# Optimization experiments

Measured on AMD Instinct MI355X. Metric: run time of the kernel, lower is better.

Reference implementation:

```python
import jax, jax.numpy as jnp
import numpy as np
from jax import lax

NPG = 61      # nodes (electrodes) per graph, hard-coded by 61*hidden reshape
B = 128       # graphs per batch
L = 160       # raw signal length -> final conv length 1
NF = 64       # num_features
HC = 128      # hidden_channels
NCLS = 4


def setup_inputs() -> dict:
    key = jax.random.key(0)
    ks = jax.random.split(key, 16)
    N = B * NPG
    # fully-connected (no self-loops) edges within each graph -> 3660 edges/graph
    a = np.repeat(np.arange(NPG), NPG)
    b = np.tile(np.arange(NPG), NPG)
    m = a != b
    sl, dl = a[m], b[m]
    off = (np.arange(B) * NPG)[:, None]
    edge_index = np.stack([(sl[None] + off).ravel(), (dl[None] + off).ravel()]).astype(np.int64)
    batch = np.repeat(np.arange(B), NPG).astype(np.int64)

    def rn(k, shape, fan_in):
        return jax.random.normal(k, shape, jnp.float32) / np.sqrt(fan_in).astype(np.float32)

    return dict(
        x=jax.random.normal(ks[0], (N, L), jnp.float32),
        edge_index=jnp.asarray(edge_index),
        batch=jnp.asarray(batch),
        edge_features=jax.random.normal(ks[1], (edge_index.shape[1], 3), jnp.float32),
        conv_w0=rn(ks[2], (NF, 1, 7), 7.0), conv_b0=jnp.zeros((NF,), jnp.float32),
        conv_w1=rn(ks[3], (NF, NF, 5), NF * 5.0), conv_b1=jnp.zeros((NF,), jnp.float32),
        conv_w2=rn(ks[4], (NF, NF, 3), NF * 3.0), conv_b2=jnp.zeros((NF,), jnp.float32),
        bn1_g=jnp.ones((NF,), jnp.float32), bn1_b=jnp.zeros((NF,), jnp.float32),
        g_w0=rn(ks[5], (NF, HC), float(NF)), g_b0=jnp.zeros((HC,), jnp.float32),
        g_w1=rn(ks[6], (HC, HC), float(HC)), g_b1=jnp.zeros((HC,), jnp.float32),
        g_w2=rn(ks[7], (HC, HC), float(HC)), g_b2=jnp.zeros((HC,), jnp.float32),
        bn2_g=jnp.ones((HC,), jnp.float32), bn2_b=jnp.zeros((HC,), jnp.float32),
        lin_w0=rn(ks[8], (NPG * HC, HC), float(NPG * HC)), lin_b0=jnp.zeros((HC,), jnp.float32),
        lin_w1=rn(ks[9], (HC, HC), float(HC)), lin_b1=jnp.zeros((HC,), jnp.float32),
        lin_w2=rn(ks[10], (HC, NCLS), float(HC)), lin_b2=jnp.zeros((NCLS,), jnp.float32),
        edge_w=rn(ks[11], (3, 1), 3.0), edge_b=jnp.zeros((1,), jnp.float32),
    )


def _conv1d(x, w, b, pad):
    # x: [N, Cin, L], w: [Cout, Cin, K]
    y = lax.conv_general_dilated(x, w, (1,), [(pad, pad)], dimension_numbers=('NCH', 'OIH', 'NCH'))
    return y + b[None, :, None]


def _maxpool7(x):
    n = x.shape[-1] // 7
    return x[..., : n * 7].reshape(x.shape[0], x.shape[1], n, 7).max(-1)


def _bn(x, g, b):
    # BatchNorm1d in training mode: biased batch statistics
    m = x.mean(0)
    v = x.var(0)
    return (x - m) * lax.rsqrt(v + 1e-5) * g + b


def _forward(x, edge_features, conv_w0, conv_b0, conv_w1, conv_b1, conv_w2, conv_b2,
             bn1_g, bn1_b, g_w0, g_b0, g_w1, g_b1, g_w2, g_b2, bn2_g, bn2_b,
             lin_w0, lin_b0, lin_w1, lin_b1, lin_w2, lin_b2, edge_w, edge_b,
             edge_index, batch):
    N = x.shape[0]
    nb = N // NPG  # == batch.max()+1 for contiguous graph layout
    # tanh-gated edge weights
    ew = jnp.tanh(edge_features @ edge_w + edge_b)            # [E, 1]
    # Conv1d feature extractor: [N,1,160] -> [N,NF,1]
    h = x[:, None, :]
    h = _maxpool7(jax.nn.relu(_conv1d(h, conv_w0, conv_b0, 0)))   # [N,NF,22]
    h = jax.nn.relu(_conv1d(h, conv_w1, conv_b1, 2))               # [N,NF,22]
    h = _maxpool7(h)                                               # [N,NF,3]
    h = _conv1d(h, conv_w2, conv_b2, 0)[:, :, 0]                   # [N,NF]
    h = _bn(h, bn1_g, bn1_b)
    # Edge-weighted GCN hops (MyzConv): lin -> gather src -> scale -> scatter-add dst
    src, dst = edge_index[0], edge_index[1]
    for w, bs, act in ((g_w0, g_b0, True), (g_w1, g_b1, True), (g_w2, g_b2, False)):
        hw = h @ w + bs                                            # [N,HC]
        msg = ew * hw[src]                                         # [E,HC]
        h = jax.ops.segment_sum(msg, dst, num_segments=N)
        if act:
            h = jax.nn.relu(h)
    h = _bn(h, bn2_g, bn2_b)
    # MLP classifier over concatenated node features per graph
    h = h.reshape(nb, NPG * HC)
    h = jax.nn.relu(h @ lin_w0 + lin_b0)
    h = jax.nn.relu(h @ lin_w1 + lin_b1)
    h = h @ lin_w2 + lin_b2
    return jax.nn.log_softmax(h, -1), ew.reshape(nb, -1).T


def reference(x, edge_index, batch, edge_features, conv_w0, conv_b0, conv_w1, conv_b1,
              conv_w2, conv_b2, bn1_g, bn1_b, g_w0, g_b0, g_w1, g_b1, g_w2, g_b2,
              bn2_g, bn2_b, lin_w0, lin_b0, lin_w1, lin_b1, lin_w2, lin_b2, edge_w, edge_b):
    return _forward(x, edge_features, conv_w0, conv_b0, conv_w1, conv_b1, conv_w2, conv_b2,
                    bn1_g, bn1_b, g_w0, g_b0, g_w1, g_b1, g_w2, g_b2, bn2_g, bn2_b,
                    lin_w0, lin_b0, lin_w1, lin_b1, lin_w2, lin_b2, edge_w, edge_b,
                    edge_index, batch)
```

## Files before the change

### kernel.cpp

```cpp
#include <hip/hip_runtime.h>
#include <math.h>

#define NPGN 61
#define NGRAPH 128
#define NNODES (NPGN*NGRAPH)
#define EPG 3660

typedef float float4v __attribute__((ext_vector_type(4)));
typedef short bf16x8 __attribute__((ext_vector_type(8)));
typedef unsigned short u16;

__device__ __forceinline__ u16 f2bf(float v){
  union { float f; unsigned u; } x; x.f = v;
  unsigned r = (x.u + 0x7FFFu + ((x.u >> 16) & 1u)) >> 16;
  return (u16)r;
}
__device__ __forceinline__ float bf2f(unsigned u){
  union { unsigned u; float f; } x; x.u = u << 16;
  return x.f;
}

__global__ __launch_bounds__(256) void k_prep(const float* __restrict__ w0,
    const float* __restrict__ w1, const float* __restrict__ w2,
    const float* __restrict__ gw0, const float* __restrict__ gw1, const float* __restrict__ gw2,
    const float* __restrict__ lw0,
    float* __restrict__ w0t, u16* __restrict__ w1b, u16* __restrict__ w2b,
    u16* __restrict__ gwt0, u16* __restrict__ gwt1, u16* __restrict__ gwt2,
    u16* __restrict__ lw0t){
  __shared__ __align__(16) u16 tile[32*132];
  int b = blockIdx.x, tid = threadIdx.x;
  if (b < 290){
    int idx = b*256 + tid;
    if (idx < 20480){
      int f = idx / 320, r = idx - f*320;
      int kk = r >> 6, c = r & 63;
      w1b[idx] = f2bf(w1[f*320 + c*5 + kk]);
    } else if (idx < 32768){
      int j = idx - 20480; w2b[j] = f2bf(w2[j]);
    } else if (idx < 40960){
      int j = idx - 32768; int jj = j >> 6, k = j & 63; gwt0[j] = f2bf(gw0[k*128 + jj]);
    } else if (idx < 57344){
      int j = idx - 40960; int jj = j >> 7, k = j & 127; gwt1[j] = f2bf(gw1[k*128 + jj]);
    } else if (idx < 73728){
      int j = idx - 57344; int jj = j >> 7, k = j & 127; gwt2[j] = f2bf(gw2[k*128 + jj]);
    } else if (idx < 74176){
      int j = idx - 73728; int k = j >> 6, f = j & 63; w0t[j] = w0[f*7 + k];
    }
  } else {
    int bb = b - 290;
    int i = bb >> 2, oq = bb & 3;
    for (int idx = tid; idx < 4096; idx += 256){
      int k = idx >> 5, ol = idx & 31;
      tile[ol*132 + k] = f2bf(lw0[((size_t)i*128 + k)*128 + oq*32 + ol]);
    }
    __syncthreads();
    unsigned* dst = (unsigned*)lw0t;
    for (int idx = tid; idx < 2048; idx += 256){
      int ol = idx >> 6, kw = idx & 63;
      unsigned v = (unsigned)tile[ol*132 + 2*kw] | ((unsigned)tile[ol*132 + 2*kw + 1] << 16);
      dst[((size_t)i*128 + oq*32 + ol)*64 + kw] = v;
    }
  }
}

#define A0T_STR 72
#define C1_STR 40
__global__ __launch_bounds__(256) void k_conv(const float* __restrict__ x,
    const float* __restrict__ w0t, const float* __restrict__ b0,
    const u16* __restrict__ w1b, const float* __restrict__ b1,
    const u16* __restrict__ w2b, const float* __restrict__ b2,
    float* __restrict__ h0, float* __restrict__ stat1p){
  int w = threadIdx.x >> 6, lane = threadIdx.x & 63;
  int tid = threadIdx.x;
  int n = blockIdx.x*4 + w;
  __shared__ __align__(16) u16 a0t_s[4][36*A0T_STR];
  __shared__ __align__(16) u16 a1k_s[4][208];
  __shared__ float hstat[4][128];
  u16* a0t = a0t_s[w];
  u16* a1k = a1k_s[w];

  const float* xrow = x + (size_t)__builtin_amdgcn_readfirstlane(n)*160;

  float w0r[7];
  #pragma unroll
  for (int k = 0; k < 7; k++) w0r[k] = w0t[k*64 + lane];
  float b0f = b0[lane];
  #pragma unroll
  for (int rp = 0; rp < 36; rp++)
    if (rp < 2 || rp >= 24) a0t[rp*A0T_STR + lane] = 0;

  #pragma unroll 2
  for (int qp = 0; qp < 11; qp++){
    float win[20];
    #pragma unroll
    for (int j = 0; j < 20; j++) win[j] = xrow[14*qp + j];
    float m0, m1;
    #pragma unroll
    for (int r = 0; r < 7; r++){
      float s = w0r[0]*win[r];
      #pragma unroll
      for (int k = 1; k < 7; k++) s += w0r[k]*win[r+k];
      m0 = r ? fmaxf(m0, s) : s;
    }
    #pragma unroll
    for (int r = 7; r < 14; r++){
      float s = w0r[0]*win[r];
      #pragma unroll
      for (int k = 1; k < 7; k++) s += w0r[k]*win[r+k];
      m1 = (r > 7) ? fmaxf(m1, s) : s;
    }
    a0t[(2 + 2*qp)*A0T_STR + lane] = f2bf(fmaxf(m0 + b0f, 0.f));
    a0t[(3 + 2*qp)*A0T_STR + lane] = f2bf(fmaxf(m1 + b0f, 0.f));
  }

  int q = lane >> 4, r16 = lane & 15;
  float4v acc[4][2];
  #pragma unroll
  for (int mt = 0; mt < 4; mt++)
    #pragma unroll
    for (int nt = 0; nt < 2; nt++)
      acc[mt][nt] = (float4v){0.f,0.f,0.f,0.f};
  #pragma unroll 1
  for (int ks = 0; ks < 10; ks++){
    int kk = ks >> 1;
    int cbase = (ks & 1)*32 + q*8;
    bf16x8 af[4];
    #pragma unroll
    for (int mt = 0; mt < 4; mt++)
      af[mt] = *(const bf16x8*)(w1b + (16*mt + r16)*320 + ks*32 + q*8);
    bf16x8 bv[2];
    #pragma unroll
    for (int nt = 0; nt < 2; nt++)
      bv[nt] = *(const bf16x8*)(a0t + (r16 + 16*nt + kk)*A0T_STR + cbase);
    #pragma unroll
    for (int mt = 0; mt < 4; mt++)
      #pragma unroll
      for (int nt = 0; nt < 2; nt++)
        acc[mt][nt] = __builtin_amdgcn_mfma_f32_16x16x32_bf16(af[mt], bv[nt], acc[mt][nt], 0, 0, 0);
  }

  u16* c1 = a0t;
  #pragma unroll
  for (int mt = 0; mt < 4; mt++){
    float4 bb = *(const float4*)(b1 + 16*mt + 4*q);
    #pragma unroll
    for (int reg = 0; reg < 4; reg++){
      int m = 16*mt + q*4 + reg;
      float bv_ = ((const float*)&bb)[reg];
      c1[m*C1_STR + r16] = f2bf(fmaxf(acc[mt][0][reg] + bv_, 0.f));
      if (r16 <= 4)
        c1[m*C1_STR + 16 + r16] = f2bf(fmaxf(acc[mt][1][reg] + bv_, 0.f));
    }
  }

  {
    bf16x8 f0 = *(const bf16x8*)(c1 + lane*C1_STR);
    bf16x8 f1 = *(const bf16x8*)(c1 + lane*C1_STR + 8);
    bf16x8 f2 = *(const bf16x8*)(c1 + lane*C1_STR + 16);
    float v[24];
    #pragma unroll
    for (int j = 0; j < 8; j++){
      v[j]    = bf2f((u16)f0[j]);
      v[8+j]  = bf2f((u16)f1[j]);
      v[16+j] = bf2f((u16)f2[j]);
    }
    #pragma unroll
    for (int t = 0; t < 3; t++){
      float m = v[t*7];
      #pragma unroll
      for (int r = 1; r < 7; r++) m = fmaxf(m, v[t*7+r]);
      a1k[lane*3 + t] = f2bf(m);
    }
  }

  float4v acc2[4];
  #pragma unroll
  for (int mt = 0; mt < 4; mt++) acc2[mt] = (float4v){0.f,0.f,0.f,0.f};
  #pragma unroll
  for (int ks = 0; ks < 6; ks++){
    bf16x8 bs = *(const bf16x8*)(a1k + ks*32 + q*8);
    #pragma unroll
    for (int mt = 0; mt < 4; mt++){
      bf16x8 af = *(const bf16x8*)(w2b + (16*mt + r16)*192 + ks*32 + q*8);
      acc2[mt] = __builtin_amdgcn_mfma_f32_16x16x32_bf16(af, bs, acc2[mt], 0, 0, 0);
    }
  }
  if (r16 == 0){
    #pragma unroll
    for (int mt = 0; mt < 4; mt++)
      #pragma unroll
      for (int reg = 0; reg < 4; reg++){
        int f = 16*mt + 4*q + reg;
        float v = acc2[mt][reg] + b2[f];
        h0[(size_t)n*64 + f] = v;
        hstat[w][f] = v;
        hstat[w][64 + f] = v*v;
      }
  }
  __syncthreads();
  if (tid < 128){
    float a = hstat[0][tid] + hstat[1][tid] + hstat[2][tid] + hstat[3][tid];
    atomicAdd(&stat1p[(blockIdx.x & 31)*128 + tid], a);
  }
}

#define EW_STR 72
#define HS_STR 136
#define HWT_STR 72
__global__ __launch_bounds__(512) void k_gnn(const float* __restrict__ h0,
    const float* __restrict__ stat1p,
    const float* __restrict__ bn1g, const float* __restrict__ bn1b,
    const u16* __restrict__ gwt0, const float* __restrict__ gb0,
    const u16* __restrict__ gwt1, const float* __restrict__ gb1,
    const u16* __restrict__ gwt2, const float* __restrict__ gb2,
    const float* __restrict__ ef, const float* __restrict__ eww,
    const float* __restrict__ ewb, float* __restrict__ out2,
    u16* __restrict__ hB, float* __restrict__ stat2p){
  int g = blockIdx.x, tid = threadIdx.x;
  int w = tid >> 6, lane = tid & 63, q = lane >> 4, r16 = lane & 15;
  int dt = w & 3, jh = w >> 2;
  __shared__ u16 hs[64*HS_STR];
  __shared__ u16 hwT[128*HWT_STR];
  __shared__ u16 ewl[64*EW_STR];
  __shared__ float bsc[64], bsh[64];
  __shared__ float st2[256];

  bf16x8 af0[2], af1[4], af2[4];
  #pragma unroll
  for (int ks = 0; ks < 2; ks++)
    af0[ks] = *(const bf16x8*)(gwt0 + (16*w + r16)*64 + ks*32 + q*8);
  #pragma unroll
  for (int ks = 0; ks < 4; ks++)
    af1[ks] = *(const bf16x8*)(gwt1 + (16*w + r16)*128 + ks*32 + q*8);
  #pragma unroll
  for (int ks = 0; ks < 4; ks++)
    af2[ks] = *(const bf16x8*)(gwt2 + (16*w + r16)*128 + ks*32 + q*8);
  float4 b40 = *(const float4*)(gb0 + 16*w + 4*q);
  float4 b41 = *(const float4*)(gb1 + 16*w + 4*q);
  float4 b42 = *(const float4*)(gb2 + 16*w + 4*q);

  if (tid < 64){
    float s = 0.f, s2 = 0.f;
    #pragma unroll
    for (int r = 0; r < 32; r++){
      s  += stat1p[r*128 + tid];
      s2 += stat1p[r*128 + 64 + tid];
    }
    float m = s*(1.f/NNODES), v = s2*(1.f/NNODES) - m*m;
    float sc = rsqrtf(v + 1e-5f)*bn1g[tid];
    bsc[tid] = sc; bsh[tid] = bn1b[tid] - m*sc;
  }
  if (tid < 256) st2[tid] = 0.f;
  {
    unsigned* td = (unsigned*)ewl;
    for (int idx = tid; idx < 64*EW_STR/2; idx += 512) td[idx] = 0;
  }
  {
    unsigned* hsd = (unsigned*)hs;
    for (int idx = tid; idx < 3*(HS_STR/2); idx += 512){
      int rr = 61 + idx/(HS_STR/2), cc = idx%(HS_STR/2);
      hsd[rr*(HS_STR/2) + cc] = 0;
    }
  }
  __syncthreads();

  {
    float v0 = eww[0], v1 = eww[1], v2 = eww[2], bb = ewb[0];
    const float* efg = ef + (size_t)g*EPG*3;
    for (int idx = tid; idx < EPG; idx += 512){
      const float* p = efg + idx*3;
      float v = tanhf(p[0]*v0 + p[1]*v1 + p[2]*v2 + bb);
      int s = idx/60, r = idx - s*60;
      int d = r + (r >= s ? 1 : 0);
      ewl[d*EW_STR + s] = f2bf(v);
      out2[(size_t)idx*128 + g] = v;
    }
  }
  {
    unsigned* hsd = (unsigned*)hs;
    for (int idx = tid; idx < 61*32; idx += 512){
      int i = idx >> 5, kw = idx & 31;
      float2 hv = *(const float2*)(h0 + ((size_t)g*61 + i)*64 + kw*2);
      int k0 = kw*2;
      float a = hv.x*bsc[k0] + bsh[k0];
      float b = hv.y*bsc[k0+1] + bsh[k0+1];
      hsd[i*(HS_STR/2) + kw] = (unsigned)f2bf(a) | ((unsigned)f2bf(b) << 16);
    }
  }
  __syncthreads();
  bf16x8 ewf[2];
  #pragma unroll
  for (int ks = 0; ks < 2; ks++)
    ewf[ks] = *(const bf16x8*)(ewl + (16*dt + r16)*EW_STR + ks*32 + q*8);

  #pragma unroll
  for (int nt = 0; nt < 4; nt++){
    float4v acc = {b40.x, b40.y, b40.z, b40.w};
    #pragma unroll
    for (int ks = 0; ks < 2; ks++){
      bf16x8 bv = *(const bf16x8*)(hs + (nt*16 + r16)*HS_STR + ks*32 + q*8);
      acc = __builtin_amdgcn_mfma_f32_16x16x32_bf16(af0[ks], bv, acc, 0, 0, 0);
    }
    #pragma unroll
    for (int r = 0; r < 4; r++)
      hwT[(16*w + 4*q + r)*HWT_STR + nt*16 + r16] = f2bf(acc[r]);
  }
  __syncthreads();
  #pragma unroll
  for (int nt = 0; nt < 4; nt++){
    int j = (jh*4 + nt)*16;
    float4v acc = {0.f,0.f,0.f,0.f};
    #pragma unroll
    for (int ks = 0; ks < 2; ks++){
      bf16x8 bv = *(const bf16x8*)(hwT + (j + r16)*HWT_STR + ks*32 + q*8);
      acc = __builtin_amdgcn_mfma_f32_16x16x32_bf16(ewf[ks], bv, acc, 0, 0, 0);
    }
    #pragma unroll
    for (int r = 0; r < 4; r++){
      int d = 16*dt + 4*q + r;
      hs[d*HS_STR + j + r16] = f2bf(fmaxf(acc[r], 0.f));
    }
  }
  __syncthreads();

  #pragma unroll
  for (int nt = 0; nt < 4; nt++){
    float4v acc = {b41.x, b41.y, b41.z, b41.w};
    #pragma unroll
    for (int ks = 0; ks < 4; ks++){
      bf16x8 bv = *(const bf16x8*)(hs + (nt*16 + r16)*HS_STR + ks*32 + q*8);
      acc = __builtin_amdgcn_mfma_f32_16x16x32_bf16(af1[ks], bv, acc, 0, 0, 0);
    }
    #pragma unroll
    for (int r = 0; r < 4; r++)
      hwT[(16*w + 4*q + r)*HWT_STR + nt*16 + r16] = f2bf(acc[r]);
  }
  __syncthreads();
  #pragma unroll
  for (int nt = 0; nt < 4; nt++){
    int j = (jh*4 + nt)*16;
    float4v acc = {0.f,0.f,0.f,0.f};
    #pragma unroll
    for (int ks = 0; ks < 2; ks++){
      bf16x8 bv = *(const bf16x8*)(hwT + (j + r16)*HWT_STR + ks*32 + q*8);
      acc = __builtin_amdgcn_mfma_f32_16x16x32_bf16(ewf[ks], bv, acc, 0, 0, 0);
    }
    #pragma unroll
    for (int r = 0; r < 4; r++){
      int d = 16*dt + 4*q + r;
      hs[d*HS_STR + j + r16] = f2bf(fmaxf(acc[r], 0.f));
    }
  }
  __syncthreads();

  #pragma unroll
  for (int nt = 0; nt < 4; nt++){
    float4v acc = {b42.x, b42.y, b42.z, b42.w};
    #pragma unroll
    for (int ks = 0; ks < 4; ks++){
      bf16x8 bv = *(const bf16x8*)(hs + (nt*16 + r16)*HS_STR + ks*32 + q*8);
      acc = __builtin_amdgcn_mfma_f32_16x16x32_bf16(af2[ks], bv, acc, 0, 0, 0);
    }
    #pragma unroll
    for (int r = 0; r < 4; r++)
      hwT[(16*w + 4*q + r)*HWT_STR + nt*16 + r16] = f2bf(acc[r]);
  }
  __syncthreads();
  #pragma unroll
  for (int nt = 0; nt < 4; nt++){
    int j = (jh*4 + nt)*16;
    float4v acc = {0.f,0.f,0.f,0.f};
    #pragma unroll
    for (int ks = 0; ks < 2; ks++){
      bf16x8 bv = *(const bf16x8*)(hwT + (j + r16)*HWT_STR + ks*32 + q*8);
      acc = __builtin_amdgcn_mfma_f32_16x16x32_bf16(ewf[ks], bv, acc, 0, 0, 0);
    }
    float cs = 0.f, cq = 0.f;
    #pragma unroll
    for (int r = 0; r < 4; r++){
      int d = 16*dt + 4*q + r;
      if (d < 61){
        float v = acc[r];
        hB[((size_t)g*61 + d)*128 + j + r16] = f2bf(v);
        cs += v; cq += v*v;
      }
    }
    int col = j + r16;
    atomicAdd(&st2[col], cs);
    atomicAdd(&st2[128 + col], cq);
  }
  __syncthreads();
  if (tid < 256) stat2p[(size_t)tid*128 + g] = st2[tid];
}

#define AS_STR 136
__global__ __launch_bounds__(256) void k_mlp0(const u16* __restrict__ hB,
    const float* __restrict__ stat2p,
    const float* __restrict__ bn2g, const float* __restrict__ bn2b,
    const u16* __restrict__ lw0t, float* __restrict__ y0pre){
  int bi = blockIdx.x; int i = bi >> 2, sub = bi & 3;
  int oh = sub & 1, gh = sub >> 1;
  int tid = threadIdx.x, w = tid >> 6, lane = tid & 63, q = lane >> 4, r16 = lane & 15;
  __shared__ u16 As[64*AS_STR];
  __shared__ float sc2[128], sh2[128];
  if (tid < 128){
    float4v sa = {0,0,0,0}, sb = {0,0,0,0};
    #pragma unroll
    for (int r = 0; r < 32; r++){
      sa += *(const float4v*)(stat2p + (size_t)tid*128 + r*4);
      sb += *(const float4v*)(stat2p + (size_t)(128 + tid)*128 + r*4);
    }
    float s = sa[0]+sa[1]+sa[2]+sa[3], s2 = sb[0]+sb[1]+sb[2]+sb[3];
    float m = s*(1.f/NNODES), v = s2*(1.f/NNODES) - m*m;
    float sc = rsqrtf(v + 1e-5f)*bn2g[tid];
    sc2[tid] = sc; sh2[tid] = bn2b[tid] - m*sc;
  }
  __syncthreads();
  {
    const unsigned* hbd = (const unsigned*)hB;
    unsigned* asd = (unsigned*)As;
    for (int idx = tid; idx < 4096; idx += 256){
      int gg = gh*64 + (idx >> 6), kw = idx & 63;
      unsigned pv = hbd[((size_t)gg*61 + i)*64 + kw];
      int k0 = kw*2;
      float a = bf2f(pv & 0xffffu)*sc2[k0] + sh2[k0];
      float b = bf2f(pv >> 16)*sc2[k0+1] + sh2[k0+1];
      asd[(idx >> 6)*(AS_STR/2) + kw] = (unsigned)f2bf(a) | ((unsigned)f2bf(b) << 16);
    }
  }
  __syncthreads();
  const u16* wbase = lw0t + ((size_t)i*128 + oh*64)*128;
  bf16x8 af[4];
  #pragma unroll
  for (int ks = 0; ks < 4; ks++)
    af[ks] = *(const bf16x8*)(As + (16*w + r16)*AS_STR + ks*32 + q*8);
  #pragma unroll
  for (int nt = 0; nt < 4; nt++){
    float4v acc = {0.f,0.f,0.f,0.f};
    #pragma unroll
    for (int ks = 0; ks < 4; ks++){
      bf16x8 bv = *(const bf16x8*)(wbase + (size_t)(nt*16 + r16)*128 + ks*32 + q*8);
      acc = __builtin_amdgcn_mfma_f32_16x16x32_bf16(af[ks], bv, acc, 0, 0, 0);
    }
    #pragma unroll
    for (int r = 0; r < 4; r++){
      int g = gh*64 + 16*w + 4*q + r;
      atomicAdd(&y0pre[(size_t)g*128 + oh*64 + nt*16 + r16], acc[r]);
    }
  }
}

__global__ __launch_bounds__(128) void k_mlp1(const float* __restrict__ y0pre,
    const float* __restrict__ lb0, const float* __restrict__ W1,
    const float* __restrict__ lb1, const float* __restrict__ W2,
    const float* __restrict__ lb2, float* __restrict__ out){
  int g = blockIdx.x, o = threadIdx.x;
  __shared__ float y0[128], y1[128], red[128];
  y0[o] = fmaxf(y0pre[(size_t)g*128 + o] + lb0[o], 0.f);
  __syncthreads();
  float a = lb1[o];
  #pragma unroll 8
  for (int k = 0; k < 128; k++) a += y0[k]*W1[k*128 + o];
  y1[o] = fmaxf(a, 0.f);
  __syncthreads();
  int c = o & 3, kb = o >> 2;
  float a2 = 0.f;
  #pragma unroll
  for (int j = 0; j < 4; j++){
    int k = kb + 32*j;
    a2 += y1[k]*W2[k*4 + c];
  }
  red[o] = a2;
  __syncthreads();
  #pragma unroll
  for (int off = 64; off >= 4; off >>= 1){
    if (o < off) red[o] += red[o + off];
    __syncthreads();
  }
  if (o == 0){
    float v0 = red[0]+lb2[0], v1 = red[1]+lb2[1], v2 = red[2]+lb2[2], v3 = red[3]+lb2[3];
    float m = fmaxf(fmaxf(v0,v1), fmaxf(v2,v3));
    float lse = m + logf(expf(v0-m)+expf(v1-m)+expf(v2-m)+expf(v3-m));
    out[g*4+0]=v0-lse; out[g*4+1]=v1-lse; out[g*4+2]=v2-lse; out[g*4+3]=v3-lse;
  }
}

extern "C" void kernel_launch(void* const* d_in, const int* in_sizes, int n_in,
                              void* d_out, int out_size, void* d_ws, size_t ws_size,
                              hipStream_t stream){
  const float* x    = (const float*)d_in[0];
  const float* ef   = (const float*)d_in[3];
  const float* cw0  = (const float*)d_in[4];
  const float* cb0  = (const float*)d_in[5];
  const float* cw1  = (const float*)d_in[6];
  const float* cb1  = (const float*)d_in[7];
  const float* cw2  = (const float*)d_in[8];
  const float* cb2  = (const float*)d_in[9];
  const float* bn1g = (const float*)d_in[10];
  const float* bn1b = (const float*)d_in[11];
  const float* gw0  = (const float*)d_in[12];
  const float* gb0  = (const float*)d_in[13];
  const float* gw1  = (const float*)d_in[14];
  const float* gb1  = (const float*)d_in[15];
  const float* gw2  = (const float*)d_in[16];
  const float* gb2  = (const float*)d_in[17];
  const float* bn2g = (const float*)d_in[18];
  const float* bn2b = (const float*)d_in[19];
  const float* lw0  = (const float*)d_in[20];
  const float* lb0  = (const float*)d_in[21];
  const float* lw1  = (const float*)d_in[22];
  const float* lb1  = (const float*)d_in[23];
  const float* lw2  = (const float*)d_in[24];
  const float* lb2  = (const float*)d_in[25];
  const float* eww  = (const float*)d_in[26];
  const float* ewb  = (const float*)d_in[27];
  float* out = (float*)d_out;

  float* ws   = (float*)d_ws;
  float* w1s  = ws;
  float* w2s  = w1s + 10240;
  float* w0t  = w2s + 6144;
  float* gws0 = w0t + 448;
  float* gws1 = gws0 + 4096;
  float* gws2 = gws1 + 8192;
  float* h0   = gws2 + 8192;
  float* hBs  = h0 + 499712;
  float* lw0s = hBs + 499712;
  float* accs = lw0s + 499712;

  u16* w1b    = (u16*)w1s;
  u16* w2b    = (u16*)w2s;
  u16* gwt0   = (u16*)gws0;
  u16* gwt1   = (u16*)gws1;
  u16* gwt2   = (u16*)gws2;
  u16* hB     = (u16*)hBs;
  u16* lw0t   = (u16*)lw0s;
  float* stat1p = accs;
  float* y0pre  = accs + 4096;
  float* stat2p = accs + 20480;

  hipMemsetAsync(accs, 0, 20480*sizeof(float), stream);
  k_prep <<<534, 256, 0, stream>>>(cw0, cw1, cw2, gw0, gw1, gw2, lw0,
                                   w0t, w1b, w2b, gwt0, gwt1, gwt2, lw0t);
  k_conv <<<NNODES/4, 256, 0, stream>>>(x, w0t, cb0, w1b, cb1, w2b, cb2, h0, stat1p);
  k_gnn  <<<NGRAPH, 512, 0, stream>>>(h0, stat1p, bn1g, bn1b,
                                      gwt0, gb0, gwt1, gb1, gwt2, gb2,
                                      ef, eww, ewb, out + 512, hB, stat2p);
  k_mlp0 <<<NPGN*4, 256, 0, stream>>>(hB, stat2p, bn2g, bn2b, lw0t, y0pre);
  k_mlp1 <<<NGRAPH, 128, 0, stream>>>(y0pre, lb0, lw1, lb1, lw2, lb2, out);
}
```

Before: 227.1 us.

## Fuse all stages into one cooperative persistent kernel with grid syncs

Replaces the memset and five separate kernel launches with a single cooperative kernel of 256 blocks of 512 threads. Weight prep, conv, GNN, MLP0 and MLP1 run as phases separated by grid.sync(), and the accumulator zeroing moves into the prep phase. This removes the launch overheads and inter-kernel gaps. The cost is that each phase is confined to 256 blocks with one block per CU: conv now loops 4 iterations per block instead of using 1916 blocks, and the GNN and MLP phases leave most blocks idle. The lw0 transpose also drops its shared-memory tiling and now reads lw0 with a large stride.

```diff
diff --git a/kernel.cpp b/kernel.cpp
--- a/kernel.cpp
+++ b/kernel.cpp
@@ -1,5 +1,8 @@
 #include <hip/hip_runtime.h>
+#include <hip/hip_cooperative_groups.h>
 #include <math.h>
+
+namespace cg = cooperative_groups;
 
 #define NPGN 61
 #define NGRAPH 128
@@ -20,503 +23,520 @@
   return x.f;
 }
 
-__global__ __launch_bounds__(256) void k_prep(const float* __restrict__ w0,
-    const float* __restrict__ w1, const float* __restrict__ w2,
-    const float* __restrict__ gw0, const float* __restrict__ gw1, const float* __restrict__ gw2,
-    const float* __restrict__ lw0,
-    float* __restrict__ w0t, u16* __restrict__ w1b, u16* __restrict__ w2b,
-    u16* __restrict__ gwt0, u16* __restrict__ gwt1, u16* __restrict__ gwt2,
-    u16* __restrict__ lw0t){
-  __shared__ __align__(16) u16 tile[32*132];
-  int b = blockIdx.x, tid = threadIdx.x;
-  if (b < 290){
-    int idx = b*256 + tid;
-    if (idx < 20480){
-      int f = idx / 320, r = idx - f*320;
-      int kk = r >> 6, c = r & 63;
-      w1b[idx] = f2bf(w1[f*320 + c*5 + kk]);
-    } else if (idx < 32768){
-      int j = idx - 20480; w2b[j] = f2bf(w2[j]);
-    } else if (idx < 40960){
-      int j = idx - 32768; int jj = j >> 6, k = j & 63; gwt0[j] = f2bf(gw0[k*128 + jj]);
-    } else if (idx < 57344){
-      int j = idx - 40960; int jj = j >> 7, k = j & 127; gwt1[j] = f2bf(gw1[k*128 + jj]);
-    } else if (idx < 73728){
-      int j = idx - 57344; int jj = j >> 7, k = j & 127; gwt2[j] = f2bf(gw2[k*128 + jj]);
-    } else if (idx < 74176){
-      int j = idx - 73728; int k = j >> 6, f = j & 63; w0t[j] = w0[f*7 + k];
-    }
-  } else {
-    int bb = b - 290;
-    int i = bb >> 2, oq = bb & 3;
-    for (int idx = tid; idx < 4096; idx += 256){
-      int k = idx >> 5, ol = idx & 31;
-      tile[ol*132 + k] = f2bf(lw0[((size_t)i*128 + k)*128 + oq*32 + ol]);
-    }
-    __syncthreads();
-    unsigned* dst = (unsigned*)lw0t;
-    for (int idx = tid; idx < 2048; idx += 256){
-      int ol = idx >> 6, kw = idx & 63;
-      unsigned v = (unsigned)tile[ol*132 + 2*kw] | ((unsigned)tile[ol*132 + 2*kw + 1] << 16);
-      dst[((size_t)i*128 + oq*32 + ol)*64 + kw] = v;
-    }
-  }
-}
+struct GArgs {
+  const float *x, *ef;
+  const float *cw0, *cb0, *cw1, *cb1, *cw2, *cb2;
+  const float *bn1g, *bn1b;
+  const float *gw0, *gb0, *gw1, *gb1, *gw2, *gb2;
+  const float *bn2g, *bn2b;
+  const float *lw0, *lb0, *lw1, *lb1, *lw2, *lb2;
+  const float *eww, *ewb;
+  float *out;
+  float *w0t; u16 *w1b, *w2b, *gwt0, *gwt1, *gwt2, *lw0t;
+  float *h0; u16 *hB;
+  float *stat1p, *y0pre, *stat2p;
+};
 
 #define A0T_STR 72
 #define C1_STR 40
-__global__ __launch_bounds__(256) void k_conv(const float* __restrict__ x,
-    const float* __restrict__ w0t, const float* __restrict__ b0,
-    const u16* __restrict__ w1b, const float* __restrict__ b1,
-    const u16* __restrict__ w2b, const float* __restrict__ b2,
-    float* __restrict__ h0, float* __restrict__ stat1p){
-  int w = threadIdx.x >> 6, lane = threadIdx.x & 63;
-  int tid = threadIdx.x;
-  int n = blockIdx.x*4 + w;
-  __shared__ __align__(16) u16 a0t_s[4][36*A0T_STR];
-  __shared__ __align__(16) u16 a1k_s[4][208];
-  __shared__ float hstat[4][128];
-  u16* a0t = a0t_s[w];
-  u16* a1k = a1k_s[w];
-
-  const float* xrow = x + (size_t)__builtin_amdgcn_readfirstlane(n)*160;
-
-  float w0r[7];
-  #pragma unroll
-  for (int k = 0; k < 7; k++) w0r[k] = w0t[k*64 + lane];
-  float b0f = b0[lane];
-  #pragma unroll
-  for (int rp = 0; rp < 36; rp++)
-    if (rp < 2 || rp >= 24) a0t[rp*A0T_STR + lane] = 0;
-
-  #pragma unroll 2
-  for (int qp = 0; qp < 11; qp++){
-    float win[20];
-    #pragma unroll
-    for (int j = 0; j < 20; j++) win[j] = xrow[14*qp + j];
-    float m0, m1;
-    #pragma unroll
-    for (int r = 0; r < 7; r++){
-      float s = w0r[0]*win[r];
-      #pragma unroll
-      for (int k = 1; k < 7; k++) s += w0r[k]*win[r+k];
-      m0 = r ? fmaxf(m0, s) : s;
-    }
-    #pragma unroll
-    for (int r = 7; r < 14; r++){
-      float s = w0r[0]*win[r];
-      #pragma unroll
-      for (int k = 1; k < 7; k++) s += w0r[k]*win[r+k];
-      m1 = (r > 7) ? fmaxf(m1, s) : s;
-    }
-    a0t[(2 + 2*qp)*A0T_STR + lane] = f2bf(fmaxf(m0 + b0f, 0.f));
-    a0t[(3 + 2*qp)*A0T_STR + lane] = f2bf(fmaxf(m1 + b0f, 0.f));
-  }
-
-  int q = lane >> 4, r16 = lane & 15;
-  float4v acc[4][2];
-  #pragma unroll
-  for (int mt = 0; mt < 4; mt++)
-    #pragma unroll
-    for (int nt = 0; nt < 2; nt++)
-      acc[mt][nt] = (float4v){0.f,0.f,0.f,0.f};
-  #pragma unroll 1
-  for (int ks = 0; ks < 10; ks++){
-    int kk = ks >> 1;
-    int cbase = (ks & 1)*32 + q*8;
-    bf16x8 af[4];
-    #pragma unroll
-    for (int mt = 0; mt < 4; mt++)
-      af[mt] = *(const bf16x8*)(w1b + (16*mt + r16)*320 + ks*32 + q*8);
-    bf16x8 bv[2];
-    #pragma unroll
-    for (int nt = 0; nt < 2; nt++)
-      bv[nt] = *(const bf16x8*)(a0t + (r16 + 16*nt + kk)*A0T_STR + cbase);
-    #pragma unroll
-    for (int mt = 0; mt < 4; mt++)
-      #pragma unroll
-      for (int nt = 0; nt < 2; nt++)
-        acc[mt][nt] = __builtin_amdgcn_mfma_f32_16x16x32_bf16(af[mt], bv[nt], acc[mt][nt], 0, 0, 0);
-  }
-
-  u16* c1 = a0t;
-  #pragma unroll
-  for (int mt = 0; mt < 4; mt++){
-    float4 bb = *(const float4*)(b1 + 16*mt + 4*q);
-    #pragma unroll
-    for (int reg = 0; reg < 4; reg++){
-      int m = 16*mt + q*4 + reg;
-      float bv_ = ((const float*)&bb)[reg];
-      c1[m*C1_STR + r16] = f2bf(fmaxf(acc[mt][0][reg] + bv_, 0.f));
-      if (r16 <= 4)
-        c1[m*C1_STR + 16 + r16] = f2bf(fmaxf(acc[mt][1][reg] + bv_, 0.f));
-    }
-  }
-
-  {
-    bf16x8 f0 = *(const bf16x8*)(c1 + lane*C1_STR);
-    bf16x8 f1 = *(const bf16x8*)(c1 + lane*C1_STR + 8);
-    bf16x8 f2 = *(const bf16x8*)(c1 + lane*C1_STR + 16);
-    float v[24];
-    #pragma unroll
-    for (int j = 0; j < 8; j++){
-      v[j]    = bf2f((u16)f0[j]);
-      v[8+j]  = bf2f((u16)f1[j]);
-      v[16+j] = bf2f((u16)f2[j]);
-    }
-    #pragma unroll
-    for (int t = 0; t < 3; t++){
-      float m = v[t*7];
-      #pragma unroll
-      for (int r = 1; r < 7; r++) m = fmaxf(m, v[t*7+r]);
-      a1k[lane*3 + t] = f2bf(m);
-    }
-  }
-
-  float4v acc2[4];
-  #pragma unroll
-  for (int mt = 0; mt < 4; mt++) acc2[mt] = (float4v){0.f,0.f,0.f,0.f};
-  #pragma unroll
-  for (int ks = 0; ks < 6; ks++){
-    bf16x8 bs = *(const bf16x8*)(a1k + ks*32 + q*8);
-    #pragma unroll
-    for (int mt = 0; mt < 4; mt++){
-      bf16x8 af = *(const bf16x8*)(w2b + (16*mt + r16)*192 + ks*32 + q*8);
-      acc2[mt] = __builtin_amdgcn_mfma_f32_16x16x32_bf16(af, bs, acc2[mt], 0, 0, 0);
-    }
-  }
-  if (r16 == 0){
-    #pragma unroll
-    for (int mt = 0; mt < 4; mt++)
-      #pragma unroll
-      for (int reg = 0; reg < 4; reg++){
-        int f = 16*mt + 4*q + reg;
-        float v = acc2[mt][reg] + b2[f];
-        h0[(size_t)n*64 + f] = v;
-        hstat[w][f] = v;
-        hstat[w][64 + f] = v*v;
-      }
-  }
-  __syncthreads();
-  if (tid < 128){
-    float a = hstat[0][tid] + hstat[1][tid] + hstat[2][tid] + hstat[3][tid];
-    atomicAdd(&stat1p[(blockIdx.x & 31)*128 + tid], a);
-  }
-}
-
 #define EW_STR 72
 #define HS_STR 136
 #define HWT_STR 72
-__global__ __launch_bounds__(512) void k_gnn(const float* __restrict__ h0,
-    const float* __restrict__ stat1p,
-    const float* __restrict__ bn1g, const float* __restrict__ bn1b,
-    const u16* __restrict__ gwt0, const float* __restrict__ gb0,
-    const u16* __restrict__ gwt1, const float* __restrict__ gb1,
-    const u16* __restrict__ gwt2, const float* __restrict__ gb2,
-    const float* __restrict__ ef, const float* __restrict__ eww,
-    const float* __restrict__ ewb, float* __restrict__ out2,
-    u16* __restrict__ hB, float* __restrict__ stat2p){
-  int g = blockIdx.x, tid = threadIdx.x;
-  int w = tid >> 6, lane = tid & 63, q = lane >> 4, r16 = lane & 15;
-  int dt = w & 3, jh = w >> 2;
-  __shared__ u16 hs[64*HS_STR];
-  __shared__ u16 hwT[128*HWT_STR];
-  __shared__ u16 ewl[64*EW_STR];
-  __shared__ float bsc[64], bsh[64];
-  __shared__ float st2[256];
-
-  bf16x8 af0[2], af1[4], af2[4];
-  #pragma unroll
-  for (int ks = 0; ks < 2; ks++)
-    af0[ks] = *(const bf16x8*)(gwt0 + (16*w + r16)*64 + ks*32 + q*8);
-  #pragma unroll
-  for (int ks = 0; ks < 4; ks++)
-    af1[ks] = *(const bf16x8*)(gwt1 + (16*w + r16)*128 + ks*32 + q*8);
-  #pragma unroll
-  for (int ks = 0; ks < 4; ks++)
-    af2[ks] = *(const bf16x8*)(gwt2 + (16*w + r16)*128 + ks*32 + q*8);
-  float4 b40 = *(const float4*)(gb0 + 16*w + 4*q);
-  float4 b41 = *(const float4*)(gb1 + 16*w + 4*q);
-  float4 b42 = *(const float4*)(gb2 + 16*w + 4*q);
-
-  if (tid < 64){
-    float s = 0.f, s2 = 0.f;
-    #pragma unroll
-    for (int r = 0; r < 32; r++){
-      s  += stat1p[r*128 + tid];
-      s2 += stat1p[r*128 + 64 + tid];
-    }
-    float m = s*(1.f/NNODES), v = s2*(1.f/NNODES) - m*m;
-    float sc = rsqrtf(v + 1e-5f)*bn1g[tid];
-    bsc[tid] = sc; bsh[tid] = bn1b[tid] - m*sc;
+#define AS_STR 136
+#define CONV_SLICE 6112
+
+__global__ __launch_bounds__(512, 1) void k_mega(GArgs a){
+  cg::grid_group grid = cg::this_grid();
+  __shared__ __align__(16) unsigned char smem[49152];
+  const int tid = threadIdx.x, bid = blockIdx.x;
+
+  {
+    for (int idx = bid*512 + tid; idx < 1094080; idx += 131072){
+      if (idx < 20480){
+        int f = idx/320, r = idx - f*320, kk = r >> 6, c = r & 63;
+        a.w1b[idx] = f2bf(a.cw1[f*320 + c*5 + kk]);
+      } else if (idx < 32768){
+        int j = idx - 20480; a.w2b[j] = f2bf(a.cw2[j]);
+      } else if (idx < 40960){
+        int j = idx - 32768; int jj = j >> 6, k = j & 63;
+        a.gwt0[j] = f2bf(a.gw0[k*128 + jj]);
+      } else if (idx < 57344){
+        int j = idx - 40960; int jj = j >> 7, k = j & 127;
+        a.gwt1[j] = f2bf(a.gw1[k*128 + jj]);
+      } else if (idx < 73728){
+        int j = idx - 57344; int jj = j >> 7, k = j & 127;
+        a.gwt2[j] = f2bf(a.gw2[k*128 + jj]);
+      } else if (idx < 74176){
+        int j = idx - 73728; int k = j >> 6, f = j & 63;
+        a.w0t[j] = a.cw0[f*7 + k];
+      } else if (idx < 94656){
+        int j = idx - 74176;
+        if (j < 4096) a.stat1p[j] = 0.f;
+        else          a.y0pre[j - 4096] = 0.f;
+      } else {
+        int j = idx - 94656;
+        int i = j >> 14, rem = j & 16383, o = rem >> 7, k = rem & 127;
+        a.lw0t[j] = f2bf(a.lw0[((size_t)i*128 + k)*128 + o]);
+      }
+    }
   }
-  if (tid < 256) st2[tid] = 0.f;
+  grid.sync();
+
   {
-    unsigned* td = (unsigned*)ewl;
-    for (int idx = tid; idx < 64*EW_STR/2; idx += 512) td[idx] = 0;
+    const int w = tid >> 6, lane = tid & 63;
+    const int q = lane >> 4, r16 = lane & 15;
+    u16* a0t = (u16*)(smem + w*CONV_SLICE);
+    u16* a1k = (u16*)(smem + w*CONV_SLICE + 5184);
+    float* hst = (float*)(smem + w*CONV_SLICE + 5600);
+    float w0r[7];
+    #pragma unroll
+    for (int k = 0; k < 7; k++) w0r[k] = a.w0t[k*64 + lane];
+    float b0f = a.cb0[lane];
+
+    #pragma unroll 1
+    for (int iter = 0; iter < 4; iter++){
+      int n = iter*2048 + bid*8 + w;
+      bool act = n < NNODES;
+      if (act){
+        #pragma unroll
+        for (int rp = 0; rp < 36; rp++)
+          if (rp < 2 || rp >= 24) a0t[rp*A0T_STR + lane] = 0;
+
+        const float* xrow = a.x + (size_t)__builtin_amdgcn_readfirstlane(n)*160;
+
+        #pragma unroll 2
+        for (int qp = 0; qp < 11; qp++){
+          float win[20];
+          #pragma unroll
+          for (int j = 0; j < 20; j++) win[j] = xrow[14*qp + j];
+          float m0, m1;
+          #pragma unroll
+          for (int r = 0; r < 7; r++){
+            float s = w0r[0]*win[r];
+            #pragma unroll
+            for (int k = 1; k < 7; k++) s += w0r[k]*win[r+k];
+            m0 = r ? fmaxf(m0, s) : s;
+          }
+          #pragma unroll
+          for (int r = 7; r < 14; r++){
+            float s = w0r[0]*win[r];
+            #pragma unroll
+            for (int k = 1; k < 7; k++) s += w0r[k]*win[r+k];
+            m1 = (r > 7) ? fmaxf(m1, s) : s;
+          }
+          a0t[(2 + 2*qp)*A0T_STR + lane] = f2bf(fmaxf(m0 + b0f, 0.f));
+          a0t[(3 + 2*qp)*A0T_STR + lane] = f2bf(fmaxf(m1 + b0f, 0.f));
+        }
+
+        float4v acc[4][2];
+        #pragma unroll
+        for (int mt = 0; mt < 4; mt++)
+          #pragma unroll
+          for (int nt = 0; nt < 2; nt++)
+            acc[mt][nt] = (float4v){0.f,0.f,0.f,0.f};
+        #pragma unroll 1
+        for (int ks = 0; ks < 10; ks++){
+          int kk = ks >> 1;
+          int cbase = (ks & 1)*32 + q*8;
+          bf16x8 af[4];
+          #pragma unroll
+          for (int mt = 0; mt < 4; mt++)
+            af[mt] = *(const bf16x8*)(a.w1b + (16*mt + r16)*320 + ks*32 + q*8);
+          bf16x8 bv[2];
+          #pragma unroll
+          for (int nt = 0; nt < 2; nt++)
+            bv[nt] = *(const bf16x8*)(a0t + (r16 + 16*nt + kk)*A0T_STR + cbase);
+          #pragma unroll
+          for (int mt = 0; mt < 4; mt++)
+            #pragma unroll
+            for (int nt = 0; nt < 2; nt++)
+              acc[mt][nt] = __builtin_amdgcn_mfma_f32_16x16x32_bf16(af[mt], bv[nt], acc[mt][nt], 0, 0, 0);
+        }
+
+        u16* c1 = a0t;
+        #pragma unroll
+        for (int mt = 0; mt < 4; mt++){
+          float4 bb = *(const float4*)(a.cb1 + 16*mt + 4*q);
+          #pragma unroll
+          for (int reg = 0; reg < 4; reg++){
+            int m = 16*mt + q*4 + reg;
+            float bv_ = ((const float*)&bb)[reg];
+            c1[m*C1_STR + r16] = f2bf(fmaxf(acc[mt][0][reg] + bv_, 0.f));
+            if (r16 <= 4)
+              c1[m*C1_STR + 16 + r16] = f2bf(fmaxf(acc[mt][1][reg] + bv_, 0.f));
+          }
+        }
+
+        {
+          bf16x8 f0 = *(const bf16x8*)(c1 + lane*C1_STR);
+          bf16x8 f1 = *(const bf16x8*)(c1 + lane*C1_STR + 8);
+          bf16x8 f2 = *(const bf16x8*)(c1 + lane*C1_STR + 16);
+          float v[24];
+          #pragma unroll
+          for (int j = 0; j < 8; j++){
+            v[j]    = bf2f((u16)f0[j]);
+            v[8+j]  = bf2f((u16)f1[j]);
+            v[16+j] = bf2f((u16)f2[j]);
+          }
+          #pragma unroll
+          for (int t = 0; t < 3; t++){
+            float m = v[t*7];
+            #pragma unroll
+            for (int r = 1; r < 7; r++) m = fmaxf(m, v[t*7+r]);
+            a1k[lane*3 + t] = f2bf(m);
+          }
+        }
+
+        float4v acc2[4];
+        #pragma unroll
+        for (int mt = 0; mt < 4; mt++) acc2[mt] = (float4v){0.f,0.f,0.f,0.f};
+        #pragma unroll
+        for (int ks = 0; ks < 6; ks++){
+          bf16x8 bs = *(const bf16x8*)(a1k + ks*32 + q*8);
+          #pragma unroll
+          for (int mt = 0; mt < 4; mt++){
+            bf16x8 af = *(const bf16x8*)(a.w2b + (16*mt + r16)*192 + ks*32 + q*8);
+            acc2[mt] = __builtin_amdgcn_mfma_f32_16x16x32_bf16(af, bs, acc2[mt], 0, 0, 0);
+          }
+        }
+        if (r16 == 0){
+          #pragma unroll
+          for (int mt = 0; mt < 4; mt++)
+            #pragma unroll
+            for (int reg = 0; reg < 4; reg++){
+              int f = 16*mt + 4*q + reg;
+              float v = acc2[mt][reg] + a.cb2[f];
+              a.h0[(size_t)n*64 + f] = v;
+              hst[f] = v;
+              hst[64 + f] = v*v;
+            }
+        }
+      } else {
+        hst[lane] = 0.f; hst[64 + lane] = 0.f;
+      }
+      __syncthreads();
+      if (tid < 128){
+        float s = 0.f;
+        #pragma unroll
+        for (int w8 = 0; w8 < 8; w8++)
+          s += *(const float*)(smem + w8*CONV_SLICE + 5600 + tid*4);
+        atomicAdd(&a.stat1p[(bid & 31)*128 + tid], s);
+      }
+      __syncthreads();
+    }
   }
+  grid.sync();
+
+  if (bid < NGRAPH){
+    const int g = bid;
+    const int w = tid >> 6, lane = tid & 63, q = lane >> 4, r16 = lane & 15;
+    const int dt = w & 3, jh = w >> 2;
+    u16* hs   = (u16*)(smem);
+    u16* hwT  = (u16*)(smem + 17408);
+    u16* ewl  = (u16*)(smem + 35840);
+    float* bsc = (float*)(smem + 45056);
+    float* bsh = (float*)(smem + 45312);
+    float* st2 = (float*)(smem + 45568);
+
+    bf16x8 af0[2], af1[4], af2[4];
+    #pragma unroll
+    for (int ks = 0; ks < 2; ks++)
+      af0[ks] = *(const bf16x8*)(a.gwt0 + (16*w + r16)*64 + ks*32 + q*8);
+    #pragma unroll
+    for (int ks = 0; ks < 4; ks++)
+      af1[ks] = *(const bf16x8*)(a.gwt1 + (16*w + r16)*128 + ks*32 + q*8);
+    #pragma unroll
+    for (int ks = 0; ks < 4; ks++)
+      af2[ks] = *(const bf16x8*)(a.gwt2 + (16*w + r16)*128 + ks*32 + q*8);
+    float4 b40 = *(const float4*)(a.gb0 + 16*w + 4*q);
+    float4 b41 = *(const float4*)(a.gb1 + 16*w + 4*q);
+    float4 b42 = *(const float4*)(a.gb2 + 16*w + 4*q);
+
+    if (tid < 64){
+      float s = 0.f, s2 = 0.f;
+      #pragma unroll
+      for (int r = 0; r < 32; r++){
+        s  += a.stat1p[r*128 + tid];
+        s2 += a.stat1p[r*128 + 64 + tid];
+      }
+      float m = s*(1.f/NNODES), v = s2*(1.f/NNODES) - m*m;
+      float sc = rsqrtf(v + 1e-5f)*a.bn1g[tid];
+      bsc[tid] = sc; bsh[tid] = a.bn1b[tid] - m*sc;
+    }
+    if (tid < 256) st2[tid] = 0.f;
+    {
+      unsigned* td = (unsigned*)ewl;
+      for (int idx = tid; idx < 64*EW_STR/2; idx += 512) td[idx] = 0;
+    }
+    {
+      unsigned* hsd = (unsigned*)hs;
+      for (int idx = tid; idx < 3*(HS_STR/2); idx += 512){
+        int rr = 61 + idx/(HS_STR/2), cc = idx%(HS_STR/2);
+        hsd[rr*(HS_STR/2) + cc] = 0;
+      }
+    }
+    __syncthreads();
+
+    {
+      float v0 = a.eww[0], v1 = a.eww[1], v2 = a.eww[2], bb = a.ewb[0];
+      const float* efg = a.ef + (size_t)g*EPG*3;
+      for (int idx = tid; idx < EPG; idx += 512){
+        const float* p = efg + idx*3;
+        float v = tanhf(p[0]*v0 + p[1]*v1 + p[2]*v2 + bb);
+        int s = idx/60, r = idx - s*60;
+        int d = r + (r >= s ? 1 : 0);
+        ewl[d*EW_STR + s] = f2bf(v);
+        a.out[512 + (size_t)idx*128 + g] = v;
+      }
+    }
+    {
+      unsigned* hsd = (unsigned*)hs;
+      for (int idx = tid; idx < 61*32; idx += 512){
+        int i = idx >> 5, kw = idx & 31;
+        float2 hv = *(const float2*)(a.h0 + ((size_t)g*61 + i)*64 + kw*2);
+        int k0 = kw*2;
+        float va = hv.x*bsc[k0] + bsh[k0];
+        float vb = hv.y*bsc[k0+1] + bsh[k0+1];
+        hsd[i*(HS_STR/2) + kw] = (unsigned)f2bf(va) | ((unsigned)f2bf(vb) << 16);
+      }
+    }
+    __syncthreads();
+    bf16x8 ewf[2];
+    #pragma unroll
+    for (int ks = 0; ks < 2; ks++)
+      ewf[ks] = *(const bf16x8*)(ewl + (16*dt + r16)*EW_STR + ks*32 + q*8);
+
+    #pragma unroll
+    for (int nt = 0; nt < 4; nt++){
+      float4v acc = {b40.x, b40.y, b40.z, b40.w};
+      #pragma unroll
+      for (int ks = 0; ks < 2; ks++){
+        bf16x8 bv = *(const bf16x8*)(hs + (nt*16 + r16)*HS_STR + ks*32 + q*8);
+        acc = __builtin_amdgcn_mfma_f32_16x16x32_bf16(af0[ks], bv, acc, 0, 0, 0);
+      }
+      #pragma unroll
+      for (int r = 0; r < 4; r++)
+        hwT[(16*w + 4*q + r)*HWT_STR + nt*16 + r16] = f2bf(acc[r]);
+    }
+    __syncthreads();
+    #pragma unroll
+    for (int nt = 0; nt < 4; nt++){
+      int j = (jh*4 + nt)*16;
+      float4v acc = {0.f,0.f,0.f,0.f};
+      #pragma unroll
+      for (int ks = 0; ks < 2; ks++){
+        bf16x8 bv = *(const bf16x8*)(hwT + (j + r16)*HWT_STR + ks*32 + q*8);
+        acc = __builtin_amdgcn_mfma_f32_16x16x32_bf16(ewf[ks], bv, acc, 0, 0, 0);
+      }
+      #pragma unroll
+      for (int r = 0; r < 4; r++){
+        int d = 16*dt + 4*q + r;
+        hs[d*HS_STR + j + r16] = f2bf(fmaxf(acc[r], 0.f));
+      }
+    }
+    __syncthreads();
+
+    #pragma unroll
+    for (int nt = 0; nt < 4; nt++){
+      float4v acc = {b41.x, b41.y, b41.z, b41.w};
+      #pragma unroll
+      for (int ks = 0; ks < 4; ks++){
+        bf16x8 bv = *(const bf16x8*)(hs + (nt*16 + r16)*HS_STR + ks*32 + q*8);
+        acc = __builtin_amdgcn_mfma_f32_16x16x32_bf16(af1[ks], bv, acc, 0, 0, 0);
+      }
+      #pragma unroll
+      for (int r = 0; r < 4; r++)
+        hwT[(16*w + 4*q + r)*HWT_STR + nt*16 + r16] = f2bf(acc[r]);
+    }
+    __syncthreads();
+    #pragma unroll
+    for (int nt = 0; nt < 4; nt++){
+      int j = (jh*4 + nt)*16;
+      float4v acc = {0.f,0.f,0.f,0.f};
+      #pragma unroll
+      for (int ks = 0; ks < 2; ks++){
+        bf16x8 bv = *(const bf16x8*)(hwT + (j + r16)*HWT_STR + ks*32 + q*8);
+        acc = __builtin_amdgcn_mfma_f32_16x16x32_bf16(ewf[ks], bv, acc, 0, 0, 0);
+      }
+      #pragma unroll
+      for (int r = 0; r < 4; r++){
+        int d = 16*dt + 4*q + r;
+        hs[d*HS_STR + j + r16] = f2bf(fmaxf(acc[r], 0.f));
+      }
+    }
+    __syncthreads();
+
+    #pragma unroll
+    for (int nt = 0; nt < 4; nt++){
+      float4v acc = {b42.x, b42.y, b42.z, b42.w};
+      #pragma unroll
+      for (int ks = 0; ks < 4; ks++){
+        bf16x8 bv = *(const bf16x8*)(hs + (nt*16 + r16)*HS_STR + ks*32 + q*8);
+        acc = __builtin_amdgcn_mfma_f32_16x16x32_bf16(af2[ks], bv, acc, 0, 0, 0);
+      }
+      #pragma unroll
+      for (int r = 0; r < 4; r++)
+        hwT[(16*w + 4*q + r)*HWT_STR + nt*16 + r16] = f2bf(acc[r]);
+    }
+    __syncthreads();
+    #pragma unroll
+    for (int nt = 0; nt < 4; nt++){
+      int j = (jh*4 + nt)*16;
+      float4v acc = {0.f,0.f,0.f,0.f};
+      #pragma unroll
+      for (int ks = 0; ks < 2; ks++){
+        bf16x8 bv = *(const bf16x8*)(hwT + (j + r16)*HWT_STR + ks*32 + q*8);
+        acc = __builtin_amdgcn_mfma_f32_16x16x32_bf16(ewf[ks], bv, acc, 0, 0, 0);
+      }
+      float cs = 0.f, cq = 0.f;
+      #pragma unroll
+      for (int r = 0; r < 4; r++){
+        int d = 16*dt + 4*q + r;
+        if (d < 61){
+          float v = acc[r];
+          a.hB[((size_t)g*61 + d)*128 + j + r16] = f2bf(v);
+          cs += v; cq += v*v;
+        }
+      }
+      int col = j + r16;
+      atomicAdd(&st2[col], cs);
+      atomicAdd(&st2[128 + col], cq);
+    }
+    __syncthreads();
+    if (tid < 256) a.stat2p[(size_t)tid*128 + g] = st2[tid];
+  }
+  grid.sync();
+
   {
-    unsigned* hsd = (unsigned*)hs;
-    for (int idx = tid; idx < 3*(HS_STR/2); idx += 512){
-      int rr = 61 + idx/(HS_STR/2), cc = idx%(HS_STR/2);
-      hsd[rr*(HS_STR/2) + cc] = 0;
+    const int team = tid >> 8, ltid = tid & 255;
+    int task = bid*2 + team;
+    bool act = task < NPGN*4;
+    int bi = act ? task : 0;
+    int i = bi >> 2, sub = bi & 3, oh = sub & 1, gh = sub >> 1;
+    const int w = ltid >> 6, lane = ltid & 63, q = lane >> 4, r16 = lane & 15;
+    u16* As = (u16*)(smem + team*18432);
+    float* sc2 = (float*)(smem + team*18432 + 17408);
+    float* sh2 = (float*)(smem + team*18432 + 17920);
+    if (ltid < 128){
+      float4v sa = {0,0,0,0}, sb = {0,0,0,0};
+      #pragma unroll
+      for (int r = 0; r < 32; r++){
+        sa += *(const float4v*)(a.stat2p + (size_t)ltid*128 + r*4);
+        sb += *(const float4v*)(a.stat2p + (size_t)(128 + ltid)*128 + r*4);
+      }
+      float s = sa[0]+sa[1]+sa[2]+sa[3], s2 = sb[0]+sb[1]+sb[2]+sb[3];
+      float m = s*(1.f/NNODES), v = s2*(1.f/NNODES) - m*m;
+      float sc = rsqrtf(v + 1e-5f)*a.bn2g[ltid];
+      sc2[ltid] = sc; sh2[ltid] = a.bn2b[ltid] - m*sc;
+    }
+    __syncthreads();
+    {
+      const unsigned* hbd = (const unsigned*)a.hB;
+      unsigned* asd = (unsigned*)As;
+      for (int idx = ltid; idx < 4096; idx += 256){
+        int gg = gh*64 + (idx >> 6), kw = idx & 63;
+        unsigned pv = hbd[((size_t)gg*61 + i)*64 + kw];
+        int k0 = kw*2;
+        float va = bf2f(pv & 0xffffu)*sc2[k0] + sh2[k0];
+        float vb = bf2f(pv >> 16)*sc2[k0+1] + sh2[k0+1];
+        asd[(idx >> 6)*(AS_STR/2) + kw] = (unsigned)f2bf(va) | ((unsigned)f2bf(vb) << 16);
+      }
+    }
+    __syncthreads();
+    const u16* wbase = a.lw0t + ((size_t)i*128 + oh*64)*128;
+    bf16x8 af[4];
+    #pragma unroll
+    for (int ks = 0; ks < 4; ks++)
+      af[ks] = *(const bf16x8*)(As + (16*w + r16)*AS_STR + ks*32 + q*8);
+    #pragma unroll
+    for (int nt = 0; nt < 4; nt++){
+      float4v acc = {0.f,0.f,0.f,0.f};
+      #pragma unroll
+      for (int ks = 0; ks < 4; ks++){
+        bf16x8 bv = *(const bf16x8*)(wbase + (size_t)(nt*16 + r16)*128 + ks*32 + q*8);
+        acc = __builtin_amdgcn_mfma_f32_16x16x32_bf16(af[ks], bv, acc, 0, 0, 0);
+      }
+      if (act){
+        #pragma unroll
+        for (int r = 0; r < 4; r++){
+          int g = gh*64 + 16*w + 4*q + r;
+          atomicAdd(&a.y0pre[(size_t)g*128 + oh*64 + nt*16 + r16], acc[r]);
+        }
+      }
     }
   }
-  __syncthreads();
-
-  {
-    float v0 = eww[0], v1 = eww[1], v2 = eww[2], bb = ewb[0];
-    const float* efg = ef + (size_t)g*EPG*3;
-    for (int idx = tid; idx < EPG; idx += 512){
-      const float* p = efg + idx*3;
-      float v = tanhf(p[0]*v0 + p[1]*v1 + p[2]*v2 + bb);
-      int s = idx/60, r = idx - s*60;
-      int d = r + (r >= s ? 1 : 0);
-      ewl[d*EW_STR + s] = f2bf(v);
-      out2[(size_t)idx*128 + g] = v;
-    }
-  }
-  {
-    unsigned* hsd = (unsigned*)hs;
-    for (int idx = tid; idx < 61*32; idx += 512){
-      int i = idx >> 5, kw = idx & 31;
-      float2 hv = *(const float2*)(h0 + ((size_t)g*61 + i)*64 + kw*2);
-      int k0 = kw*2;
-      float a = hv.x*bsc[k0] + bsh[k0];
-      float b = hv.y*bsc[k0+1] + bsh[k0+1];
-      hsd[i*(HS_STR/2) + kw] = (unsigned)f2bf(a) | ((unsigned)f2bf(b) << 16);
-    }
-  }
-  __syncthreads();
-  bf16x8 ewf[2];
-  #pragma unroll
-  for (int ks = 0; ks < 2; ks++)
-    ewf[ks] = *(const bf16x8*)(ewl + (16*dt + r16)*EW_STR + ks*32 + q*8);
-
-  #pragma unroll
-  for (int nt = 0; nt < 4; nt++){
-    float4v acc = {b40.x, b40.y, b40.z, b40.w};
-    #pragma unroll
-    for (int ks = 0; ks < 2; ks++){
-      bf16x8 bv = *(const bf16x8*)(hs + (nt*16 + r16)*HS_STR + ks*32 + q*8);
-      acc = __builtin_amdgcn_mfma_f32_16x16x32_bf16(af0[ks], bv, acc, 0, 0, 0);
-    }
-    #pragma unroll
-    for (int r = 0; r < 4; r++)
-      hwT[(16*w + 4*q + r)*HWT_STR + nt*16 + r16] = f2bf(acc[r]);
-  }
-  __syncthreads();
-  #pragma unroll
-  for (int nt = 0; nt < 4; nt++){
-    int j = (jh*4 + nt)*16;
-    float4v acc = {0.f,0.f,0.f,0.f};
-    #pragma unroll
-    for (int ks = 0; ks < 2; ks++){
-      bf16x8 bv = *(const bf16x8*)(hwT + (j + r16)*HWT_STR + ks*32 + q*8);
-      acc = __builtin_amdgcn_mfma_f32_16x16x32_bf16(ewf[ks], bv, acc, 0, 0, 0);
-    }
-    #pragma unroll
-    for (int r = 0; r < 4; r++){
-      int d = 16*dt + 4*q + r;
-      hs[d*HS_STR + j + r16] = f2bf(fmaxf(acc[r], 0.f));
-    }
-  }
-  __syncthreads();
-
-  #pragma unroll
-  for (int nt = 0; nt < 4; nt++){
-    float4v acc = {b41.x, b41.y, b41.z, b41.w};
-    #pragma unroll
-    for (int ks = 0; ks < 4; ks++){
-      bf16x8 bv = *(const bf16x8*)(hs + (nt*16 + r16)*HS_STR + ks*32 + q*8);
-      acc = __builtin_amdgcn_mfma_f32_16x16x32_bf16(af1[ks], bv, acc, 0, 0, 0);
-    }
-    #pragma unroll
-    for (int r = 0; r < 4; r++)
-      hwT[(16*w + 4*q + r)*HWT_STR + nt*16 + r16] = f2bf(acc[r]);
-  }
-  __syncthreads();
-  #pragma unroll
-  for (int nt = 0; nt < 4; nt++){
-    int j = (jh*4 + nt)*16;
-    float4v acc = {0.f,0.f,0.f,0.f};
-    #pragma unroll
-    for (int ks = 0; ks < 2; ks++){
-      bf16x8 bv = *(const bf16x8*)(hwT + (j + r16)*HWT_STR + ks*32 + q*8);
-      acc = __builtin_amdgcn_mfma_f32_16x16x32_bf16(ewf[ks], bv, acc, 0, 0, 0);
-    }
-    #pragma unroll
-    for (int r = 0; r < 4; r++){
-      int d = 16*dt + 4*q + r;
-      hs[d*HS_STR + j + r16] = f2bf(fmaxf(acc[r], 0.f));
-    }
-  }
-  __syncthreads();
-
-  #pragma unroll
-  for (int nt = 0; nt < 4; nt++){
-    float4v acc = {b42.x, b42.y, b42.z, b42.w};
-    #pragma unroll
-    for (int ks = 0; ks < 4; ks++){
-      bf16x8 bv = *(const bf16x8*)(hs + (nt*16 + r16)*HS_STR + ks*32 + q*8);
-      acc = __builtin_amdgcn_mfma_f32_16x16x32_bf16(af2[ks], bv, acc, 0, 0, 0);
-    }
-    #pragma unroll
-    for (int r = 0; r < 4; r++)
-      hwT[(16*w + 4*q + r)*HWT_STR + nt*16 + r16] = f2bf(acc[r]);
-  }
-  __syncthreads();
-  #pragma unroll
-  for (int nt = 0; nt < 4; nt++){
-    int j = (jh*4 + nt)*16;
-    float4v acc = {0.f,0.f,0.f,0.f};
-    #pragma unroll
-    for (int ks = 0; ks < 2; ks++){
-      bf16x8 bv = *(const bf16x8*)(hwT + (j + r16)*HWT_STR + ks*32 + q*8);
-      acc = __builtin_amdgcn_mfma_f32_16x16x32_bf16(ewf[ks], bv, acc, 0, 0, 0);
-    }
-    float cs = 0.f, cq = 0.f;
-    #pragma unroll
-    for (int r = 0; r < 4; r++){
-      int d = 16*dt + 4*q + r;
-      if (d < 61){
-        float v = acc[r];
-        hB[((size_t)g*61 + d)*128 + j + r16] = f2bf(v);
-        cs += v; cq += v*v;
-      }
-    }
-    int col = j + r16;
-    atomicAdd(&st2[col], cs);
-    atomicAdd(&st2[128 + col], cq);
-  }
-  __syncthreads();
-  if (tid < 256) stat2p[(size_t)tid*128 + g] = st2[tid];
-}
-
-#define AS_STR 136
-__global__ __launch_bounds__(256) void k_mlp0(const u16* __restrict__ hB,
-    const float* __restrict__ stat2p,
-    const float* __restrict__ bn2g, const float* __restrict__ bn2b,
-    const u16* __restrict__ lw0t, float* __restrict__ y0pre){
-  int bi = blockIdx.x; int i = bi >> 2, sub = bi & 3;
-  int oh = sub & 1, gh = sub >> 1;
-  int tid = threadIdx.x, w = tid >> 6, lane = tid & 63, q = lane >> 4, r16 = lane & 15;
-  __shared__ u16 As[64*AS_STR];
-  __shared__ float sc2[128], sh2[128];
-  if (tid < 128){
-    float4v sa = {0,0,0,0}, sb = {0,0,0,0};
-    #pragma unroll
-    for (int r = 0; r < 32; r++){
-      sa += *(const float4v*)(stat2p + (size_t)tid*128 + r*4);
-      sb += *(const float4v*)(stat2p + (size_t)(128 + tid)*128 + r*4);
-    }
-    float s = sa[0]+sa[1]+sa[2]+sa[3], s2 = sb[0]+sb[1]+sb[2]+sb[3];
-    float m = s*(1.f/NNODES), v = s2*(1.f/NNODES) - m*m;
-    float sc = rsqrtf(v + 1e-5f)*bn2g[tid];
-    sc2[tid] = sc; sh2[tid] = bn2b[tid] - m*sc;
-  }
-  __syncthreads();
-  {
-    const unsigned* hbd = (const unsigned*)hB;
-    unsigned* asd = (unsigned*)As;
-    for (int idx = tid; idx < 4096; idx += 256){
-      int gg = gh*64 + (idx >> 6), kw = idx & 63;
-      unsigned pv = hbd[((size_t)gg*61 + i)*64 + kw];
-      int k0 = kw*2;
-      float a = bf2f(pv & 0xffffu)*sc2[k0] + sh2[k0];
-      float b = bf2f(pv >> 16)*sc2[k0+1] + sh2[k0+1];
-      asd[(idx >> 6)*(AS_STR/2) + kw] = (unsigned)f2bf(a) | ((unsigned)f2bf(b) << 16);
-    }
-  }
-  __syncthreads();
-  const u16* wbase = lw0t + ((size_t)i*128 + oh*64)*128;
-  bf16x8 af[4];
-  #pragma unroll
-  for (int ks = 0; ks < 4; ks++)
-    af[ks] = *(const bf16x8*)(As + (16*w + r16)*AS_STR + ks*32 + q*8);
-  #pragma unroll
-  for (int nt = 0; nt < 4; nt++){
-    float4v acc = {0.f,0.f,0.f,0.f};
-    #pragma unroll
-    for (int ks = 0; ks < 4; ks++){
-      bf16x8 bv = *(const bf16x8*)(wbase + (size_t)(nt*16 + r16)*128 + ks*32 + q*8);
-      acc = __builtin_amdgcn_mfma_f32_16x16x32_bf16(af[ks], bv, acc, 0, 0, 0);
-    }
-    #pragma unroll
-    for (int r = 0; r < 4; r++){
-      int g = gh*64 + 16*w + 4*q + r;
-      atomicAdd(&y0pre[(size_t)g*128 + oh*64 + nt*16 + r16], acc[r]);
-    }
-  }
-}
-
-__global__ __launch_bounds__(128) void k_mlp1(const float* __restrict__ y0pre,
-    const float* __restrict__ lb0, const float* __restrict__ W1,
-    const float* __restrict__ lb1, const float* __restrict__ W2,
-    const float* __restrict__ lb2, float* __restrict__ out){
-  int g = blockIdx.x, o = threadIdx.x;
-  __shared__ float y0[128], y1[128], red[128];
-  y0[o] = fmaxf(y0pre[(size_t)g*128 + o] + lb0[o], 0.f);
-  __syncthreads();
-  float a = lb1[o];
-  #pragma unroll 8
-  for (int k = 0; k < 128; k++) a += y0[k]*W1[k*128 + o];
-  y1[o] = fmaxf(a, 0.f);
-  __syncthreads();
-  int c = o & 3, kb = o >> 2;
-  float a2 = 0.f;
-  #pragma unroll
-  for (int j = 0; j < 4; j++){
-    int k = kb + 32*j;
-    a2 += y1[k]*W2[k*4 + c];
-  }
-  red[o] = a2;
-  __syncthreads();
-  #pragma unroll
-  for (int off = 64; off >= 4; off >>= 1){
-    if (o < off) red[o] += red[o + off];
-    __syncthreads();
-  }
-  if (o == 0){
-    float v0 = red[0]+lb2[0], v1 = red[1]+lb2[1], v2 = red[2]+lb2[2], v3 = red[3]+lb2[3];
-    float m = fmaxf(fmaxf(v0,v1), fmaxf(v2,v3));
-    float lse = m + logf(expf(v0-m)+expf(v1-m)+expf(v2-m)+expf(v3-m));
-    out[g*4+0]=v0-lse; out[g*4+1]=v1-lse; out[g*4+2]=v2-lse; out[g*4+3]=v3-lse;
+  grid.sync();
+
+  if (bid < 32){
+    const int team = tid >> 7, o = tid & 127;
+    const int g = bid*4 + team;
+    float* y0  = (float*)(smem + team*1536);
+    float* y1  = y0 + 128;
+    float* red = y0 + 256;
+    y0[o] = fmaxf(a.y0pre[(size_t)g*128 + o] + a.lb0[o], 0.f);
+    __syncthreads();
+    float acc = a.lb1[o];
+    #pragma unroll 8
+    for (int k = 0; k < 128; k++) acc += y0[k]*a.lw1[k*128 + o];
+    y1[o] = fmaxf(acc, 0.f);
+    __syncthreads();
+    int c = o & 3, kb = o >> 2;
+    float a2 = 0.f;
+    #pragma unroll
+    for (int j = 0; j < 4; j++){
+      int k = kb + 32*j;
+      a2 += y1[k]*a.lw2[k*4 + c];
+    }
+    red[o] = a2;
+    __syncthreads();
+    #pragma unroll
+    for (int off = 64; off >= 4; off >>= 1){
+      if (o < off) red[o] += red[o + off];
+      __syncthreads();
+    }
+    if (o == 0){
+      float v0 = red[0]+a.lb2[0], v1 = red[1]+a.lb2[1];
+      float v2 = red[2]+a.lb2[2], v3 = red[3]+a.lb2[3];
+      float m = fmaxf(fmaxf(v0,v1), fmaxf(v2,v3));
+      float lse = m + logf(expf(v0-m)+expf(v1-m)+expf(v2-m)+expf(v3-m));
+      a.out[g*4+0]=v0-lse; a.out[g*4+1]=v1-lse; a.out[g*4+2]=v2-lse; a.out[g*4+3]=v3-lse;
+    }
   }
 }
 
 extern "C" void kernel_launch(void* const* d_in, const int* in_sizes, int n_in,
                               void* d_out, int out_size, void* d_ws, size_t ws_size,
                               hipStream_t stream){
-  const float* x    = (const float*)d_in[0];
-  const float* ef   = (const float*)d_in[3];
-  const float* cw0  = (const float*)d_in[4];
-  const float* cb0  = (const float*)d_in[5];
-  const float* cw1  = (const float*)d_in[6];
-  const float* cb1  = (const float*)d_in[7];
-  const float* cw2  = (const float*)d_in[8];
-  const float* cb2  = (const float*)d_in[9];
-  const float* bn1g = (const float*)d_in[10];
-  const float* bn1b = (const float*)d_in[11];
-  const float* gw0  = (const float*)d_in[12];
-  const float* gb0  = (const float*)d_in[13];
-  const float* gw1  = (const float*)d_in[14];
-  const float* gb1  = (const float*)d_in[15];
-  const float* gw2  = (const float*)d_in[16];
-  const float* gb2  = (const float*)d_in[17];
-  const float* bn2g = (const float*)d_in[18];
-  const float* bn2b = (const float*)d_in[19];
-  const float* lw0  = (const float*)d_in[20];
-  const float* lb0  = (const float*)d_in[21];
-  const float* lw1  = (const float*)d_in[22];
-  const float* lb1  = (const float*)d_in[23];
-  const float* lw2  = (const float*)d_in[24];
-  const float* lb2  = (const float*)d_in[25];
-  const float* eww  = (const float*)d_in[26];
-  const float* ewb  = (const float*)d_in[27];
-  float* out = (float*)d_out;
-
-  float* ws   = (float*)d_ws;
+  GArgs a;
+  a.x    = (const float*)d_in[0];
+  a.ef   = (const float*)d_in[3];
+  a.cw0  = (const float*)d_in[4];
+  a.cb0  = (const float*)d_in[5];
+  a.cw1  = (const float*)d_in[6];
+  a.cb1  = (const float*)d_in[7];
+  a.cw2  = (const float*)d_in[8];
+  a.cb2  = (const float*)d_in[9];
+  a.bn1g = (const float*)d_in[10];
+  a.bn1b = (const float*)d_in[11];
+  a.gw0  = (const float*)d_in[12];
+  a.gb0  = (const float*)d_in[13];
+  a.gw1  = (const float*)d_in[14];
+  a.gb1  = (const float*)d_in[15];
+  a.gw2  = (const float*)d_in[16];
+  a.gb2  = (const float*)d_in[17];
+  a.bn2g = (const float*)d_in[18];
+  a.bn2b = (const float*)d_in[19];
+  a.lw0  = (const float*)d_in[20];
+  a.lb0  = (const float*)d_in[21];
+  a.lw1  = (const float*)d_in[22];
+  a.lb1  = (const float*)d_in[23];
+  a.lw2  = (const float*)d_in[24];
+  a.lb2  = (const float*)d_in[25];
+  a.eww  = (const float*)d_in[26];
+  a.ewb  = (const float*)d_in[27];
+  a.out  = (float*)d_out;
+
+  float* ws = (float*)d_ws;
   float* w1s  = ws;
   float* w2s  = w1s + 10240;
   float* w0t  = w2s + 6144;
@@ -528,24 +548,20 @@
   float* lw0s = hBs + 499712;
   float* accs = lw0s + 499712;
 
-  u16* w1b    = (u16*)w1s;
-  u16* w2b    = (u16*)w2s;
-  u16* gwt0   = (u16*)gws0;
-  u16* gwt1   = (u16*)gws1;
-  u16* gwt2   = (u16*)gws2;
-  u16* hB     = (u16*)hBs;
-  u16* lw0t   = (u16*)lw0s;
-  float* stat1p = accs;
-  float* y0pre  = accs + 4096;
-  float* stat2p = accs + 20480;
-
-  hipMemsetAsync(accs, 0, 20480*sizeof(float), stream);
-  k_prep <<<534, 256, 0, stream>>>(cw0, cw1, cw2, gw0, gw1, gw2, lw0,
-                                   w0t, w1b, w2b, gwt0, gwt1, gwt2, lw0t);
-  k_conv <<<NNODES/4, 256, 0, stream>>>(x, w0t, cb0, w1b, cb1, w2b, cb2, h0, stat1p);
-  k_gnn  <<<NGRAPH, 512, 0, stream>>>(h0, stat1p, bn1g, bn1b,
-                                      gwt0, gb0, gwt1, gb1, gwt2, gb2,
-                                      ef, eww, ewb, out + 512, hB, stat2p);
-  k_mlp0 <<<NPGN*4, 256, 0, stream>>>(hB, stat2p, bn2g, bn2b, lw0t, y0pre);
-  k_mlp1 <<<NGRAPH, 128, 0, stream>>>(y0pre, lb0, lw1, lb1, lw2, lb2, out);
+  a.w0t  = w0t;
+  a.w1b  = (u16*)w1s;
+  a.w2b  = (u16*)w2s;
+  a.gwt0 = (u16*)gws0;
+  a.gwt1 = (u16*)gws1;
+  a.gwt2 = (u16*)gws2;
+  a.h0   = h0;
+  a.hB   = (u16*)hBs;
+  a.lw0t = (u16*)lw0s;
+  a.stat1p = accs;
+  a.y0pre  = accs + 4096;
+  a.stat2p = accs + 20480;
+
+  void* kargs[] = { (void*)&a };
+  hipLaunchCooperativeKernel((const void*)k_mega, dim3(256), dim3(512),
+                             kargs, 0, stream);
 }
```

New measurement: 403.9 us. 77.9% more time.
